# Performance work log

Hardware: AMD Instinct MI355X
Metric: run time of the kernel (lower is better)

## Reference

```python
import jax, jax.numpy as jnp
import numpy as np

B, S, V, D, F, H, L = 2, 1024, 32000, 768, 3072, 12, 6
DH = D // H


def layer_norm(x, g, b, eps=1e-5):
    mu = jnp.mean(x, axis=-1, keepdims=True)
    var = jnp.mean((x - mu) ** 2, axis=-1, keepdims=True)
    return (x - mu) / jnp.sqrt(var + eps) * g + b


def setup_inputs() -> dict:
    key = jax.random.key(0)
    ks = jax.random.split(key, 20)
    s = 0.02  # init scale
    p = {
        'x': jax.random.randint(ks[0], (B, S), 0, V),
        'tok_emb': jax.random.normal(ks[1], (V, D), jnp.float32) * s,
        'pos_emb': jax.random.normal(ks[2], (S, D), jnp.float32) * s,
        'Wq': jax.random.normal(ks[3], (L, D, D), jnp.float32) * s,
        'bq': jnp.zeros((L, D), jnp.float32),
        'Wk': jax.random.normal(ks[4], (L, D, D), jnp.float32) * s,
        'bk': jnp.zeros((L, D), jnp.float32),
        'Wv': jax.random.normal(ks[5], (L, D, D), jnp.float32) * s,
        'bv': jnp.zeros((L, D), jnp.float32),
        'Wo': jax.random.normal(ks[6], (L, D, D), jnp.float32) * s,
        'bo': jnp.zeros((L, D), jnp.float32),
        'ln1_g': jnp.ones((L, D), jnp.float32),
        'ln1_b': jnp.zeros((L, D), jnp.float32),
        'W1': jax.random.normal(ks[7], (L, D, F), jnp.float32) * s,
        'b1': jnp.zeros((L, F), jnp.float32),
        'W2': jax.random.normal(ks[8], (L, F, D), jnp.float32) * s,
        'b2': jnp.zeros((L, D), jnp.float32),
        'ln2_g': jnp.ones((L, D), jnp.float32),
        'ln2_b': jnp.zeros((L, D), jnp.float32),
        'Wf': jax.random.normal(ks[9], (D, V), jnp.float32) * s,
        'bf': jnp.zeros((V,), jnp.float32),
    }
    return p


def reference(x, tok_emb, pos_emb, Wq, bq, Wk, bk, Wv, bv, Wo, bo,
              ln1_g, ln1_b, W1, b1, W2, b2, ln2_g, ln2_b, Wf, bf):
    hset = tok_emb[x] + pos_emb[None, :x.shape[1], :]  # [B,S,D]
    scale = 1.0 / jnp.sqrt(jnp.float32(D))  # note: original scales by sqrt(d_k)=sqrt(d_model)
    for i in range(L):
        q = (hset @ Wq[i] + bq[i]).reshape(B, S, H, DH).transpose(0, 2, 1, 3)
        k = (hset @ Wk[i] + bk[i]).reshape(B, S, H, DH).transpose(0, 2, 1, 3)
        v = (hset @ Wv[i] + bv[i]).reshape(B, S, H, DH).transpose(0, 2, 1, 3)
        scores = jnp.einsum('bhqd,bhkd->bhqk', q, k) * scale
        probs = jax.nn.softmax(scores, axis=-1)
        o = jnp.einsum('bhqk,bhkd->bhqd', probs, v)
        o = o.transpose(0, 2, 1, 3).reshape(B, S, D)
        attn = o @ Wo[i] + bo[i]
        h1 = layer_norm(attn + hset, ln1_g[i], ln1_b[i])
        ff = jax.nn.gelu(h1 @ W1[i] + b1[i], approximate=False) @ W2[i] + b2[i]
        hset = layer_norm(ff + h1, ln2_g[i], ln2_b[i])
    logits = hset @ Wf + bf
    log_probs = jax.nn.log_softmax(logits, axis=-1)
    return (log_probs, hset)
```

## Files before the change

### kernel.cpp

```cpp
#include <hip/hip_runtime.h>
#include <hip/hip_bf16.h>
#include <math.h>

#define B_ 2
#define S_ 1024
#define V_ 32000
#define D_ 768
#define F_ 3072
#define H_ 12
#define L_ 6
#define DH_ 64
#define BS_ (B_*S_)
#define NQKV_ 2304
#define KVB_ 128

typedef __attribute__((ext_vector_type(8))) short short8;
typedef __attribute__((ext_vector_type(4))) float f32x4;

__device__ __forceinline__ unsigned short f2b(float f) {
    union { __hip_bfloat16 h; unsigned short u; } cv;
    cv.h = __float2bfloat16(f);
    return cv.u;
}

__device__ __forceinline__ void store_bf4(__hip_bfloat16* p, float a, float b, float c, float d) {
    unsigned long long pk = (unsigned long long)f2b(a)
        | ((unsigned long long)f2b(b) << 16)
        | ((unsigned long long)f2b(c) << 32)
        | ((unsigned long long)f2b(d) << 48);
    *(unsigned long long*)p = pk;
}

__device__ __forceinline__ void gld16(const void* g, void* l) {
    __builtin_amdgcn_global_load_lds(
        (const __attribute__((address_space(1))) unsigned int*)g,
        (__attribute__((address_space(3))) unsigned int*)l,
        16, 0, 0);
}

__global__ void embed_k(const int* __restrict__ x, const float* __restrict__ tok,
                        const float* __restrict__ pos, float* __restrict__ h,
                        __hip_bfloat16* __restrict__ hbf) {
    int bs = blockIdx.x;
    int s = bs % S_;
    int t = x[bs];
    for (int d = threadIdx.x; d < D_; d += blockDim.x) {
        float v = tok[(size_t)t * D_ + d] + pos[(size_t)s * D_ + d];
        h[(size_t)bs * D_ + d] = v;
        hbf[(size_t)bs * D_ + d] = __float2bfloat16(v);
    }
}

__global__ __launch_bounds__(256) void transp_k(const float* __restrict__ src, size_t sl,
                                                __hip_bfloat16* __restrict__ dst, size_t dl,
                                                int N, int K) {
    const float* S = src + (size_t)blockIdx.z * sl;
    __hip_bfloat16* Dp = dst + (size_t)blockIdx.z * dl;
    __shared__ float T[32][33];
    const int k0 = blockIdx.y * 32, n0 = blockIdx.x * 32;
    const int tid = threadIdx.x;
    const int r = tid >> 3, c4 = (tid & 7) * 4;
    float4 vv = *(const float4*)&S[(size_t)(k0 + r) * N + n0 + c4];
    T[r][c4 + 0] = vv.x; T[r][c4 + 1] = vv.y; T[r][c4 + 2] = vv.z; T[r][c4 + 3] = vv.w;
    __syncthreads();
    store_bf4(&Dp[(size_t)(n0 + r) * K + k0 + c4],
              T[c4 + 0][r], T[c4 + 1][r], T[c4 + 2][r], T[c4 + 3][r]);
}

__global__ void bcat_k(const float* __restrict__ bq, const float* __restrict__ bk,
                       const float* __restrict__ bv, float* __restrict__ dst) {
    int l = blockIdx.x;
    for (int j = threadIdx.x; j < D_; j += blockDim.x) {
        dst[(size_t)l * NQKV_ + j]          = bq[(size_t)l * D_ + j];
        dst[(size_t)l * NQKV_ + D_ + j]     = bk[(size_t)l * D_ + j];
        dst[(size_t)l * NQKV_ + 2 * D_ + j] = bv[(size_t)l * D_ + j];
    }
}

template<int BM, int BN, int ACT, bool WF32, bool WBF, bool SW, bool XS, bool WVT>
__global__ __launch_bounds__(256) void mgemm_k(const __hip_bfloat16* __restrict__ A,
                                               const __hip_bfloat16* __restrict__ Bt,
                                               const float* __restrict__ bias,
                                               float* __restrict__ Cf,
                                               __hip_bfloat16* __restrict__ Cb,
                                               __hip_bfloat16* __restrict__ vTp,
                                               int M, int N, int K) {
    constexpr int WM = BM / 2, WN = BN / 2;
    constexpr int FM = WM / 16, FN = WN / 16;
    __shared__ __hip_bfloat16 Al[BM * 64];
    __shared__ __hip_bfloat16 Bl[BN * 64];
    const int tid = threadIdx.x;
    const int wid = tid >> 6, lane = tid & 63;
    const int wr = wid >> 1, wc = wid & 1;
    const int lrow = lane & 15, kq = lane >> 4;

    int bx = blockIdx.x, by = blockIdx.y;
    if (XS) {
        const int gx = gridDim.x;
        const int nwg = gx * gridDim.y;
        const int lin = by * gx + bx;
        const int logical = (lin & 7) * (nwg >> 3) + (lin >> 3);
        bx = logical % gx;
        by = logical / gx;
    }
    const int row0 = (SW ? bx : by) * BM;
    const int col0 = (SW ? by : bx) * BN;

    f32x4 acc[FM][FN];
    #pragma unroll
    for (int i = 0; i < FM; ++i)
        #pragma unroll
        for (int j = 0; j < FN; ++j)
            acc[i][j] = (f32x4){0.f, 0.f, 0.f, 0.f};

    const int srow = (lane >> 3);
    const int scol = ((lane & 7) ^ srow) * 8;

    for (int kk = 0; kk < K; kk += 64) {
        #pragma unroll
        for (int i = 0; i < BM / 32; ++i)
            gld16(A + (size_t)(row0 + i * 32 + wid * 8 + srow) * K + kk + scol,
                  &Al[(i * 32 + wid * 8) * 64]);
        #pragma unroll
        for (int i = 0; i < BN / 32; ++i)
            gld16(Bt + (size_t)(col0 + i * 32 + wid * 8 + srow) * K + kk + scol,
                  &Bl[(i * 32 + wid * 8) * 64]);
        __syncthreads();

        #pragma unroll
        for (int kc = 0; kc < 2; ++kc) {
            short8 af[FM], bfr[FN];
            #pragma unroll
            for (int i = 0; i < FM; ++i) {
                const int row = wr * WM + i * 16 + lrow;
                af[i] = *(const short8*)((const char*)Al + row * 128
                          + ((kc * 64 + kq * 16) ^ ((row & 7) << 4)));
            }
            #pragma unroll
            for (int j = 0; j < FN; ++j) {
                const int row = wc * WN + j * 16 + lrow;
                bfr[j] = *(const short8*)((const char*)Bl + row * 128
                          + ((kc * 64 + kq * 16) ^ ((row & 7) << 4)));
            }
            #pragma unroll
            for (int i = 0; i < FM; ++i)
                #pragma unroll
                for (int j = 0; j < FN; ++j)
                    acc[i][j] = __builtin_amdgcn_mfma_f32_16x16x32_bf16(af[i], bfr[j], acc[i][j], 0, 0, 0);
        }
        __syncthreads();
    }

    #pragma unroll
    for (int i = 0; i < FM; ++i)
        #pragma unroll
        for (int j = 0; j < FN; ++j) {
            const int col = col0 + wc * WN + j * 16 + lrow;
            const float bv = bias[col];
            const int rowq = row0 + wr * WM + i * 16 + kq * 4;
            if (WVT && col >= 1536) {
                const int cv = col - 1536;
                const int bh = (rowq >> 10) * H_ + (cv >> 6);
                store_bf4(&vTp[((size_t)bh * DH_ + (cv & 63)) * S_ + (rowq & 1023)],
                          acc[i][j][0] + bv, acc[i][j][1] + bv,
                          acc[i][j][2] + bv, acc[i][j][3] + bv);
            } else {
                #pragma unroll
                for (int r = 0; r < 4; ++r) {
                    const int row = rowq + r;
                    float vv = acc[i][j][r] + bv;
                    if (ACT == 1) vv = 0.5f * vv * (1.0f + erff(vv * 0.70710678118654752f));
                    if (WVT && col < D_) vv *= 0.03608439182435161f;
                    if (WF32) Cf[(size_t)row * N + col] = vv;
                    if (WBF)  Cb[(size_t)row * N + col] = __float2bfloat16(vv);
                }
            }
        }
}

__global__ __launch_bounds__(256) void gemm_k(const float* __restrict__ A,
                                              const float* __restrict__ W,
                                              const float* __restrict__ bias,
                                              float* __restrict__ Cout,
                                              int M, int N, int K) {
    __shared__ float As[64][16];
    __shared__ float Bs[16][64];
    const int tid = threadIdx.x;
    const int tx = tid & 15, ty = tid >> 4;
    const int row0 = blockIdx.y * 64, col0 = blockIdx.x * 64;
    float acc[4][4] = {};

    for (int kk = 0; kk < K; kk += 16) {
        #pragma unroll
        for (int it = 0; it < 4; ++it) {
            int idx = tid + it * 256;
            int m = idx >> 4, k = idx & 15;
            As[m][k] = A[(size_t)(row0 + m) * K + kk + k];
            int r = idx >> 6, c = idx & 63;
            Bs[r][c] = W[(size_t)(kk + r) * N + col0 + c];
        }
        __syncthreads();
        #pragma unroll
        for (int k = 0; k < 16; ++k) {
            float a[4], b[4];
            #pragma unroll
            for (int i = 0; i < 4; ++i) a[i] = As[ty * 4 + i][k];
            #pragma unroll
            for (int j = 0; j < 4; ++j) b[j] = Bs[k][tx * 4 + j];
            #pragma unroll
            for (int i = 0; i < 4; ++i)
                #pragma unroll
                for (int j = 0; j < 4; ++j)
                    acc[i][j] += a[i] * b[j];
        }
        __syncthreads();
    }

    #pragma unroll
    for (int i = 0; i < 4; ++i) {
        int r = row0 + ty * 4 + i;
        #pragma unroll
        for (int j = 0; j < 4; ++j) {
            int c = col0 + tx * 4 + j;
            Cout[(size_t)r * N + c] = acc[i][j] + bias[c];
        }
    }
}

__global__ __launch_bounds__(256) void fattn_k(const __hip_bfloat16* __restrict__ qkv,
                                               const __hip_bfloat16* __restrict__ vT,
                                               __hip_bfloat16* __restrict__ o) {
    const int qt0 = blockIdx.x * 64;
    const int bh = blockIdx.y;
    const int b = bh / H_, hh = bh % H_;
    const size_t rb = (size_t)b * S_;
    const int hoff = hh * DH_;

    __shared__ __hip_bfloat16 Ks[2][KVB_ * 64];
    __shared__ __hip_bfloat16 Vt[2][64 * KVB_];
    __shared__ __hip_bfloat16 Ps[64 * KVB_];

    const int tid = threadIdx.x;
    const int w = tid >> 6, lane = tid & 63;
    const int lr = lane & 15, lk = lane >> 4;
    const size_t vbase = (size_t)bh * DH_ * S_;

    short8 aq[2];
    {
        const int qrow = qt0 + w * 16 + lr;
        #pragma unroll
        for (int kc = 0; kc < 2; ++kc)
            aq[kc] = *(const short8*)&qkv[(rb + qrow) * NQKV_ + hoff + kc * 32 + lk * 8];
    }

    f32x4 oacc[4];
    float m_i[4], l_i[4];
    #pragma unroll
    for (int r = 0; r < 4; ++r) {
        oacc[r] = (f32x4){0.f, 0.f, 0.f, 0.f};
        m_i[r] = -1e30f;
        l_i[r] = 0.f;
    }

    auto stage = [&](int bi, int kt0) {
        #pragma unroll
        for (int t = 0; t < 4; ++t) {
            const int r0 = w * 32 + t * 8;
            const int r = r0 + (lane >> 3);
            const int cs = (lane & 7) ^ ((r & 7) ^ ((r >> 3) & 7));
            gld16(&qkv[(rb + kt0 + r) * NQKV_ + D_ + hoff + cs * 8], &Ks[bi][r0 * 64]);
        }
        #pragma unroll
        for (int t = 0; t < 4; ++t) {
            const int d0 = w * 16 + t * 4;
            const int d = d0 + (lane >> 4);
            const int cs = (lane & 15) ^ (d & 15);
            gld16(&vT[vbase + (size_t)d * S_ + kt0 + cs * 8], &Vt[bi][d0 * 128]);
        }
    };

    stage(0, 0);
    int cur = 0;
    for (int kt0 = 0; kt0 < S_; kt0 += KVB_) {
        __syncthreads();
        if (kt0 + KVB_ < S_) stage(cur ^ 1, kt0 + KVB_);
        const char* Kb = (const char*)Ks[cur];
        const char* Vb = (const char*)Vt[cur];

        f32x4 s[8];
        #pragma unroll
        for (int j = 0; j < 8; ++j) s[j] = (f32x4){0.f, 0.f, 0.f, 0.f};
        __builtin_amdgcn_s_setprio(1);
        #pragma unroll
        for (int kc = 0; kc < 2; ++kc) {
            #pragma unroll
            for (int j = 0; j < 8; ++j) {
                int kr = j * 16 + lr;
                short8 bk = *(const short8*)(Kb + kr * 128
                              + ((kc * 64 + lk * 16) ^ ((((kr & 7) ^ ((kr >> 3) & 7)) << 4))));
                s[j] = __builtin_amdgcn_mfma_f32_16x16x32_bf16(aq[kc], bk, s[j], 0, 0, 0);
            }
        }
        __builtin_amdgcn_s_setprio(0);

        #pragma unroll
        for (int r = 0; r < 4; ++r) {
            float tmax = s[0][r];
            #pragma unroll
            for (int j = 1; j < 8; ++j) tmax = fmaxf(tmax, s[j][r]);
            #pragma unroll
            for (int off = 1; off <= 8; off <<= 1)
                tmax = fmaxf(tmax, __shfl_xor(tmax, off));
            float mnew = fmaxf(m_i[r], tmax);
            float corr = __expf(m_i[r] - mnew);
            m_i[r] = mnew;
            float psum = 0.f;
            const int prow = w * 16 + lk * 4 + r;
            #pragma unroll
            for (int j = 0; j < 8; ++j) {
                float p = __expf(s[j][r] - mnew);
                psum += p;
                *(__hip_bfloat16*)((char*)Ps + prow * 256
                    + (((j * 16 + lr) * 2) ^ ((prow & 15) << 4))) = __float2bfloat16(p);
            }
            #pragma unroll
            for (int off = 1; off <= 8; off <<= 1)
                psum += __shfl_xor(psum, off);
            l_i[r] = l_i[r] * corr + psum;
            #pragma unroll
            for (int jd = 0; jd < 4; ++jd) oacc[jd][r] *= corr;
        }

        __builtin_amdgcn_s_setprio(1);
        #pragma unroll
        for (int ks = 0; ks < 4; ++ks) {
            const int prow = w * 16 + lr;
            short8 pa = *(const short8*)((const char*)Ps + prow * 256
                          + ((ks * 64 + lk * 16) ^ ((prow & 15) << 4)));
            #pragma unroll
            for (int jd = 0; jd < 4; ++jd) {
                int vr = jd * 16 + lr;
                short8 vb = *(const short8*)(Vb + vr * 256
                              + ((ks * 64 + lk * 16) ^ ((vr & 15) << 4)));
                oacc[jd] = __builtin_amdgcn_mfma_f32_16x16x32_bf16(pa, vb, oacc[jd], 0, 0, 0);
            }
        }
        __builtin_amdgcn_s_setprio(0);
        cur ^= 1;
    }

    #pragma unroll
    for (int r = 0; r < 4; ++r) {
        float inv = 1.0f / l_i[r];
        const int row = qt0 + w * 16 + lk * 4 + r;
        #pragma unroll
        for (int jd = 0; jd < 4; ++jd)
            o[(rb + row) * (size_t)D_ + hoff + jd * 16 + lr] = __float2bfloat16(oacc[jd][r] * inv);
    }
}

__global__ __launch_bounds__(256) void addln_k(const float* __restrict__ a,
                                               const float* __restrict__ b,
                                               const float* __restrict__ g,
                                               const float* __restrict__ beta,
                                               float* __restrict__ out,
                                               __hip_bfloat16* __restrict__ out_bf) {
    const int r = blockIdx.x;
    const int tid = threadIdx.x;
    __shared__ float red[256];
    float xv[3];
    float s = 0.f;
    #pragma unroll
    for (int i = 0; i < 3; ++i) {
        int d = tid + i * 256;
        xv[i] = a[(size_t)r * D_ + d] + b[(size_t)r * D_ + d];
        s += xv[i];
    }
    red[tid] = s; __syncthreads();
    for (int st = 128; st > 0; st >>= 1) { if (tid < st) red[tid] += red[tid + st]; __syncthreads(); }
    float mu = red[0] * (1.0f / D_);
    __syncthreads();
    s = 0.f;
    #pragma unroll
    for (int i = 0; i < 3; ++i) { float dd = xv[i] - mu; s += dd * dd; }
    red[tid] = s; __syncthreads();
    for (int st = 128; st > 0; st >>= 1) { if (tid < st) red[tid] += red[tid + st]; __syncthreads(); }
    float rstd = rsqrtf(red[0] * (1.0f / D_) + 1e-5f);
    #pragma unroll
    for (int i = 0; i < 3; ++i) {
        int d = tid + i * 256;
        float v = (xv[i] - mu) * rstd * g[d] + beta[d];
        out[(size_t)r * D_ + d] = v;
        out_bf[(size_t)r * D_ + d] = __float2bfloat16(v);
    }
}

__global__ __launch_bounds__(256) void lsm_k(float* __restrict__ lp) {
    const int r = blockIdx.x;
    const int tid = threadIdx.x;
    __shared__ float rm[256], rl[256];
    float* row = lp + (size_t)r * V_;
    float mt = -1e30f, lt = 0.f;
    for (int i = tid * 4; i < V_; i += 1024) {
        float4 v = *(const float4*)&row[i];
        float c = fmaxf(fmaxf(v.x, v.y), fmaxf(v.z, v.w));
        if (c > mt) { lt *= __expf(mt - c); mt = c; }
        lt += __expf(v.x - mt) + __expf(v.y - mt) + __expf(v.z - mt) + __expf(v.w - mt);
    }
    rm[tid] = mt; rl[tid] = lt; __syncthreads();
    for (int st = 128; st > 0; st >>= 1) {
        if (tid < st) {
            float m2 = rm[tid + st], l2 = rl[tid + st];
            float M = fmaxf(rm[tid], m2);
            rl[tid] = rl[tid] * __expf(rm[tid] - M) + l2 * __expf(m2 - M);
            rm[tid] = M;
        }
        __syncthreads();
    }
    float sub = rm[0] + __logf(rl[0]);
    for (int i = tid * 4; i < V_; i += 1024) {
        float4 v = *(const float4*)&row[i];
        v.x -= sub; v.y -= sub; v.z -= sub; v.w -= sub;
        *(float4*)&row[i] = v;
    }
}

extern "C" void kernel_launch(void* const* d_in, const int* in_sizes, int n_in,
                              void* d_out, int out_size, void* d_ws, size_t ws_size,
                              hipStream_t stream) {
    const int*   x    = (const int*)  d_in[0];
    const float* tok  = (const float*)d_in[1];
    const float* pos  = (const float*)d_in[2];
    const float* Wq   = (const float*)d_in[3];
    const float* bq   = (const float*)d_in[4];
    const float* Wk   = (const float*)d_in[5];
    const float* bk   = (const float*)d_in[6];
    const float* Wv   = (const float*)d_in[7];
    const float* bv   = (const float*)d_in[8];
    const float* Wo   = (const float*)d_in[9];
    const float* bo   = (const float*)d_in[10];
    const float* ln1g = (const float*)d_in[11];
    const float* ln1b = (const float*)d_in[12];
    const float* W1   = (const float*)d_in[13];
    const float* b1   = (const float*)d_in[14];
    const float* W2   = (const float*)d_in[15];
    const float* b2   = (const float*)d_in[16];
    const float* ln2g = (const float*)d_in[17];
    const float* ln2b = (const float*)d_in[18];
    const float* Wf   = (const float*)d_in[19];
    const float* bff  = (const float*)d_in[20];

    float* out = (float*)d_out;
    const size_t HS = (size_t)BS_ * D_;

    __hip_bfloat16* qkv_bf = (__hip_bfloat16*)out;
    __hip_bfloat16* vT     = (__hip_bfloat16*)(out + 2359296);
    __hip_bfloat16* att_bf = (__hip_bfloat16*)(out + 4718592);
    float* tmp   = out + 5505024;
    float* h1    = out + 7077888;
    __hip_bfloat16* h1_bf  = (__hip_bfloat16*)(out + 8650752);
    __hip_bfloat16* ff_bf  = (__hip_bfloat16*)(out + 9437184);
    __hip_bfloat16* h_bf   = (__hip_bfloat16*)(out + 12582912);
    __hip_bfloat16* Wqkv_t = (__hip_bfloat16*)(out + 13369344);
    __hip_bfloat16* Wo_t   = (__hip_bfloat16*)(out + 18677760);
    __hip_bfloat16* W1_t   = (__hip_bfloat16*)(out + 20447232);
    __hip_bfloat16* W2_t   = (__hip_bfloat16*)(out + 27525120);
    float* bqkv  = out + 34603008;
    float* h     = out + (size_t)BS_ * V_;

    const bool ws_ok = ws_size >= 52297728ULL;
    __hip_bfloat16* Wf_t   = (__hip_bfloat16*)d_ws;
    __hip_bfloat16* hbf_ws = (__hip_bfloat16*)((char*)d_ws + 49152000);

    const size_t DD = (size_t)D_ * D_, DF = (size_t)D_ * F_;
    const size_t QKVL = (size_t)NQKV_ * D_;
    transp_k<<<dim3(D_/32, D_/32, L_), 256, 0, stream>>>(Wq, DD, Wqkv_t,          QKVL, D_, D_);
    transp_k<<<dim3(D_/32, D_/32, L_), 256, 0, stream>>>(Wk, DD, Wqkv_t + DD,     QKVL, D_, D_);
    transp_k<<<dim3(D_/32, D_/32, L_), 256, 0, stream>>>(Wv, DD, Wqkv_t + 2 * DD, QKVL, D_, D_);
    transp_k<<<dim3(D_/32, D_/32, L_), 256, 0, stream>>>(Wo, DD, Wo_t,            DD,   D_, D_);
    transp_k<<<dim3(F_/32, D_/32, L_), 256, 0, stream>>>(W1, DF, W1_t,            DF,   F_, D_);
    transp_k<<<dim3(D_/32, F_/32, L_), 256, 0, stream>>>(W2, DF, W2_t,            DF,   D_, F_);
    bcat_k<<<L_, 256, 0, stream>>>(bq, bk, bv, bqkv);
    if (ws_ok)
        transp_k<<<dim3(V_/32, D_/32, 1), 256, 0, stream>>>(Wf, 0, Wf_t, 0, V_, D_);

    embed_k<<<BS_, 256, 0, stream>>>(x, tok, pos, h, h_bf);

    const dim3 gQKV(NQKV_/128, BS_/128);
    const dim3 gFF1(F_/128,    BS_/128);
    const dim3 gOUT64(D_/64,   BS_/64);
    const dim3 gA(S_/64, B_*H_);
    for (int i = 0; i < L_; ++i) {
        mgemm_k<128,128,0,false,true,false,false,true><<<gQKV, 256, 0, stream>>>(
            h_bf, Wqkv_t + (size_t)i * QKVL, bqkv + (size_t)i * NQKV_, nullptr, qkv_bf, vT, BS_, NQKV_, D_);
        fattn_k<<<gA, 256, 0, stream>>>(qkv_bf, vT, att_bf);
        mgemm_k<64,64,0,true,false,false,false,false><<<gOUT64, 256, 0, stream>>>(
            att_bf, Wo_t + (size_t)i * DD, bo + (size_t)i * D_, tmp, nullptr, nullptr, BS_, D_, D_);
        addln_k<<<BS_, 256, 0, stream>>>(tmp, h, ln1g + (size_t)i * D_, ln1b + (size_t)i * D_, h1, h1_bf);
        mgemm_k<128,128,1,false,true,false,false,false><<<gFF1, 256, 0, stream>>>(
            h1_bf, W1_t + (size_t)i * DF, b1 + (size_t)i * F_, nullptr, ff_bf, nullptr, BS_, F_, D_);
        mgemm_k<64,64,0,true,false,false,false,false><<<gOUT64, 256, 0, stream>>>(
            ff_bf, W2_t + (size_t)i * DF, b2 + (size_t)i * D_, tmp, nullptr, nullptr, BS_, D_, F_);
        __hip_bfloat16* obf = (i == L_ - 1 && ws_ok) ? hbf_ws : h_bf;
        addln_k<<<BS_, 256, 0, stream>>>(tmp, h1, ln2g + (size_t)i * D_, ln2b + (size_t)i * D_, h, obf);
    }

    if (ws_ok) {
        mgemm_k<128,128,0,true,false,true,true,false><<<dim3(BS_/128, V_/128), 256, 0, stream>>>(
            hbf_ws, Wf_t, bff, out, nullptr, nullptr, BS_, V_, D_);
    } else {
        gemm_k<<<dim3(V_/64, BS_/64), 256, 0, stream>>>(h, Wf, bff, out, BS_, V_, D_);
    }
    lsm_k<<<BS_, 256, 0, stream>>>(out);
}
```

Before: 1.247 ms.

## Add lazy softmax rescaling, warp-shuffle reductions, and smaller GEMM M-tiles

Flash attention now skips the max-shuffle and accumulator rescale unless some row's new tile maximum exceeds the running max by more than 8, letting exponentials grow up to e^8 before renormalizing. The layer-norm and log-softmax kernels replace shared-memory tree reductions with wave shuffles plus a four-entry cross-wave combine, and layer norm computes mean and variance in a single pass using E[x^2]-mu^2. The QKV and FF1 GEMMs move to 64x128 tiles, doubling the block count to improve CU occupancy. The changes trade some numerical robustness (single-pass variance, deferred rescaling) for fewer syncs and fewer instructions.

```diff
diff --git a/kernel.cpp b/kernel.cpp
--- a/kernel.cpp
+++ b/kernel.cpp
@@ -303,22 +303,38 @@
         }
         __builtin_amdgcn_s_setprio(0);
 
+        float tmax[4];
         #pragma unroll
         for (int r = 0; r < 4; ++r) {
-            float tmax = s[0][r];
-            #pragma unroll
-            for (int j = 1; j < 8; ++j) tmax = fmaxf(tmax, s[j][r]);
-            #pragma unroll
-            for (int off = 1; off <= 8; off <<= 1)
-                tmax = fmaxf(tmax, __shfl_xor(tmax, off));
-            float mnew = fmaxf(m_i[r], tmax);
-            float corr = __expf(m_i[r] - mnew);
-            m_i[r] = mnew;
+            float t = s[0][r];
+            #pragma unroll
+            for (int j = 1; j < 8; ++j) t = fmaxf(t, s[j][r]);
+            tmax[r] = t;
+        }
+        float excess = fmaxf(fmaxf(tmax[0] - m_i[0], tmax[1] - m_i[1]),
+                             fmaxf(tmax[2] - m_i[2], tmax[3] - m_i[3]));
+        if (!__all(excess <= 8.0f)) {
+            #pragma unroll
+            for (int r = 0; r < 4; ++r) {
+                float tm = tmax[r];
+                #pragma unroll
+                for (int off = 1; off <= 8; off <<= 1)
+                    tm = fmaxf(tm, __shfl_xor(tm, off));
+                float mnew = fmaxf(m_i[r], tm);
+                float corr = __expf(m_i[r] - mnew);
+                m_i[r] = mnew;
+                l_i[r] *= corr;
+                #pragma unroll
+                for (int jd = 0; jd < 4; ++jd) oacc[jd][r] *= corr;
+            }
+        }
+        #pragma unroll
+        for (int r = 0; r < 4; ++r) {
             float psum = 0.f;
             const int prow = w * 16 + lk * 4 + r;
             #pragma unroll
             for (int j = 0; j < 8; ++j) {
-                float p = __expf(s[j][r] - mnew);
+                float p = __expf(s[j][r] - m_i[r]);
                 psum += p;
                 *(__hip_bfloat16*)((char*)Ps + prow * 256
                     + (((j * 16 + lr) * 2) ^ ((prow & 15) << 4))) = __float2bfloat16(p);
@@ -326,9 +342,7 @@
             #pragma unroll
             for (int off = 1; off <= 8; off <<= 1)
                 psum += __shfl_xor(psum, off);
-            l_i[r] = l_i[r] * corr + psum;
-            #pragma unroll
-            for (int jd = 0; jd < 4; ++jd) oacc[jd][r] *= corr;
+            l_i[r] += psum;
         }
 
         __builtin_amdgcn_s_setprio(1);
@@ -367,25 +381,29 @@
                                                __hip_bfloat16* __restrict__ out_bf) {
     const int r = blockIdx.x;
     const int tid = threadIdx.x;
-    __shared__ float red[256];
+    const int wid = tid >> 6, lane = tid & 63;
+    __shared__ float w1[4], w2[4];
     float xv[3];
-    float s = 0.f;
+    float s1 = 0.f, s2 = 0.f;
     #pragma unroll
     for (int i = 0; i < 3; ++i) {
         int d = tid + i * 256;
         xv[i] = a[(size_t)r * D_ + d] + b[(size_t)r * D_ + d];
-        s += xv[i];
-    }
-    red[tid] = s; __syncthreads();
-    for (int st = 128; st > 0; st >>= 1) { if (tid < st) red[tid] += red[tid + st]; __syncthreads(); }
-    float mu = red[0] * (1.0f / D_);
+        s1 += xv[i];
+        s2 += xv[i] * xv[i];
+    }
+    #pragma unroll
+    for (int off = 1; off <= 32; off <<= 1) {
+        s1 += __shfl_xor(s1, off);
+        s2 += __shfl_xor(s2, off);
+    }
+    if (lane == 0) { w1[wid] = s1; w2[wid] = s2; }
     __syncthreads();
-    s = 0.f;
-    #pragma unroll
-    for (int i = 0; i < 3; ++i) { float dd = xv[i] - mu; s += dd * dd; }
-    red[tid] = s; __syncthreads();
-    for (int st = 128; st > 0; st >>= 1) { if (tid < st) red[tid] += red[tid + st]; __syncthreads(); }
-    float rstd = rsqrtf(red[0] * (1.0f / D_) + 1e-5f);
+    s1 = w1[0] + w1[1] + w1[2] + w1[3];
+    s2 = w2[0] + w2[1] + w2[2] + w2[3];
+    float mu = s1 * (1.0f / D_);
+    float var = s2 * (1.0f / D_) - mu * mu;
+    float rstd = rsqrtf(var + 1e-5f);
     #pragma unroll
     for (int i = 0; i < 3; ++i) {
         int d = tid + i * 256;
@@ -398,7 +416,8 @@
 __global__ __launch_bounds__(256) void lsm_k(float* __restrict__ lp) {
     const int r = blockIdx.x;
     const int tid = threadIdx.x;
-    __shared__ float rm[256], rl[256];
+    const int wid = tid >> 6, lane = tid & 63;
+    __shared__ float wm[4], wl[4];
     float* row = lp + (size_t)r * V_;
     float mt = -1e30f, lt = 0.f;
     for (int i = tid * 4; i < V_; i += 1024) {
@@ -407,17 +426,19 @@
         if (c > mt) { lt *= __expf(mt - c); mt = c; }
         lt += __expf(v.x - mt) + __expf(v.y - mt) + __expf(v.z - mt) + __expf(v.w - mt);
     }
-    rm[tid] = mt; rl[tid] = lt; __syncthreads();
-    for (int st = 128; st > 0; st >>= 1) {
-        if (tid < st) {
-            float m2 = rm[tid + st], l2 = rl[tid + st];
-            float M = fmaxf(rm[tid], m2);
-            rl[tid] = rl[tid] * __expf(rm[tid] - M) + l2 * __expf(m2 - M);
-            rm[tid] = M;
-        }
-        __syncthreads();
-    }
-    float sub = rm[0] + __logf(rl[0]);
+    #pragma unroll
+    for (int off = 1; off <= 32; off <<= 1) {
+        float m2 = __shfl_xor(mt, off), l2 = __shfl_xor(lt, off);
+        float M = fmaxf(mt, m2);
+        lt = lt * __expf(mt - M) + l2 * __expf(m2 - M);
+        mt = M;
+    }
+    if (lane == 0) { wm[wid] = mt; wl[wid] = lt; }
+    __syncthreads();
+    float M4 = fmaxf(fmaxf(wm[0], wm[1]), fmaxf(wm[2], wm[3]));
+    float L4 = wl[0] * __expf(wm[0] - M4) + wl[1] * __expf(wm[1] - M4)
+             + wl[2] * __expf(wm[2] - M4) + wl[3] * __expf(wm[3] - M4);
+    float sub = M4 + __logf(L4);
     for (int i = tid * 4; i < V_; i += 1024) {
         float4 v = *(const float4*)&row[i];
         v.x -= sub; v.y -= sub; v.z -= sub; v.w -= sub;
@@ -486,18 +507,18 @@
 
     embed_k<<<BS_, 256, 0, stream>>>(x, tok, pos, h, h_bf);
 
-    const dim3 gQKV(NQKV_/128, BS_/128);
-    const dim3 gFF1(F_/128,    BS_/128);
+    const dim3 gQKV(NQKV_/128, BS_/64);
+    const dim3 gFF1(F_/128,    BS_/64);
     const dim3 gOUT64(D_/64,   BS_/64);
     const dim3 gA(S_/64, B_*H_);
     for (int i = 0; i < L_; ++i) {
-        mgemm_k<128,128,0,false,true,false,false,true><<<gQKV, 256, 0, stream>>>(
+        mgemm_k<64,128,0,false,true,false,false,true><<<gQKV, 256, 0, stream>>>(
             h_bf, Wqkv_t + (size_t)i * QKVL, bqkv + (size_t)i * NQKV_, nullptr, qkv_bf, vT, BS_, NQKV_, D_);
         fattn_k<<<gA, 256, 0, stream>>>(qkv_bf, vT, att_bf);
         mgemm_k<64,64,0,true,false,false,false,false><<<gOUT64, 256, 0, stream>>>(
             att_bf, Wo_t + (size_t)i * DD, bo + (size_t)i * D_, tmp, nullptr, nullptr, BS_, D_, D_);
         addln_k<<<BS_, 256, 0, stream>>>(tmp, h, ln1g + (size_t)i * D_, ln1b + (size_t)i * D_, h1, h1_bf);
-        mgemm_k<128,128,1,false,true,false,false,false><<<gFF1, 256, 0, stream>>>(
+        mgemm_k<64,128,1,false,true,false,false,false><<<gFF1, 256, 0, stream>>>(
             h1_bf, W1_t + (size_t)i * DF, b1 + (size_t)i * F_, nullptr, ff_bf, nullptr, BS_, F_, D_);
         mgemm_k<64,64,0,true,false,false,false,false><<<gOUT64, 256, 0, stream>>>(
             ff_bf, W2_t + (size_t)i * DF, b2 + (size_t)i * D_, tmp, nullptr, nullptr, BS_, D_, F_);
```

New measurement: 1.163 ms. 1.07x faster.
